# Optimization experiments

Measured on AMD Instinct MI355X. Metric: run time of the kernel, lower is better.

The kernel has to match this reference:

```python
import jax, jax.numpy as jnp
import numpy as np

B, N, D = 4, 2048, 1024
H = 16
HD = D // H


def setup_inputs() -> dict:
    key = jax.random.key(0)
    ks = jax.random.split(key, 7)
    bound_w = 1.0 / np.sqrt(D)  # kaiming_uniform(a=sqrt(5)) on (D, D) -> U(-1/sqrt(fan_in), 1/sqrt(fan_in))
    x = jax.random.normal(ks[0], (B, N, D), dtype=jnp.float32)
    Wq = jax.random.uniform(ks[1], (D, D), jnp.float32, -bound_w, bound_w)
    Wk = jax.random.uniform(ks[2], (D, D), jnp.float32, -bound_w, bound_w)
    Wv = jax.random.uniform(ks[3], (D, D), jnp.float32, -bound_w, bound_w)
    Wo = jax.random.uniform(ks[4], (D, D), jnp.float32, -bound_w, bound_w)
    bo = jax.random.uniform(ks[5], (D,), jnp.float32, -bound_w, bound_w)
    return {"x": x, "Wq": Wq, "Wk": Wk, "Wv": Wv, "Wo": Wo, "bo": bo}


def reference(x, Wq, Wk, Wv, Wo, bo):
    b, n, _ = x.shape
    # QKV projections: contraction over W's FIRST axis, matching torch einsum 'bnd,di->bni'
    Q = jnp.einsum('bnd,di->bni', x, Wq)
    K = jnp.einsum('bnd,di->bni', x, Wk)
    V = jnp.einsum('bnd,di->bni', x, Wv)
    # split heads: [b, h, n, hd]
    Q = Q.reshape(b, n, H, HD).transpose(0, 2, 1, 3)
    K = K.reshape(b, n, H, HD).transpose(0, 2, 1, 3)
    V = V.reshape(b, n, H, HD).transpose(0, 2, 1, 3)
    scores = jnp.einsum('bhnd,bhmd->bhnm', Q, K) / np.sqrt(HD).astype(np.float32)
    causal = jnp.triu(jnp.ones((n, n), dtype=bool), k=1)  # True above diagonal -> masked
    scores = jnp.where(causal[None, None, :, :], -jnp.inf, scores)
    attn = jax.nn.softmax(scores, axis=-1)
    # dropout rate is 0.0 -> identity
    ctx = jnp.einsum('bhnm,bhmd->bhnd', attn, V)
    ctx = ctx.transpose(0, 2, 1, 3).reshape(b, n, D)
    return ctx @ Wo.T + bo
```

## Files before the change

kernel.cpp:

```cpp
#include <hip/hip_runtime.h>
#include <hip/hip_bf16.h>

typedef __bf16 bf16;
typedef __bf16 bf16x4 __attribute__((ext_vector_type(4)));
typedef __bf16 bf16x8 __attribute__((ext_vector_type(8)));
typedef float  f32x4  __attribute__((ext_vector_type(4)));

#define B_  4
#define N_  2048
#define D_  1024
#define H_  16
#define HD_ 64

#define QSCALE 0.1803368801111204f

__device__ __forceinline__ bf16x8 ld8(const bf16* p) {
  return *reinterpret_cast<const bf16x8*>(p);
}
__device__ __forceinline__ float max3f(float a, float b, float c) {
  return fmaxf(fmaxf(a, b), c);
}

__device__ __forceinline__ void gload16(const bf16* g, bf16* l) {
  __builtin_amdgcn_global_load_lds(
      (const __attribute__((address_space(1))) void*)g,
      (__attribute__((address_space(3))) void*)l, 16, 0, 0);
}

__global__ __launch_bounds__(256) void cast_k(const float* __restrict__ in,
                                              bf16* __restrict__ out, int n) {
  int i = (blockIdx.x * 256 + threadIdx.x) * 8;
  if (i >= n) return;
  float4 a = *reinterpret_cast<const float4*>(in + i);
  float4 b = *reinterpret_cast<const float4*>(in + i + 4);
  bf16x8 o;
  o[0] = (bf16)a.x; o[1] = (bf16)a.y; o[2] = (bf16)a.z; o[3] = (bf16)a.w;
  o[4] = (bf16)b.x; o[5] = (bf16)b.y; o[6] = (bf16)b.z; o[7] = (bf16)b.w;
  *reinterpret_cast<bf16x8*>(out + i) = o;
}

__global__ __launch_bounds__(1024)
void transpose3_k(const float* __restrict__ w0, const float* __restrict__ w1,
                  const float* __restrict__ w2, bf16* __restrict__ out) {
  __shared__ float t[32][33];
  const int z = blockIdx.z;
  const float* in = (z == 0) ? w0 : (z == 1) ? w1 : w2;
  const float scale = (z == 0) ? QSCALE : 1.0f;
  bf16* o = out + (size_t)z * D_ * D_;
  int c = blockIdx.x * 32 + threadIdx.x;
  int r = blockIdx.y * 32 + threadIdx.y;
  t[threadIdx.y][threadIdx.x] = in[r * D_ + c];
  __syncthreads();
  int oc = blockIdx.y * 32 + threadIdx.x;
  int orr = blockIdx.x * 32 + threadIdx.y;
  o[orr * D_ + oc] = (bf16)(scale * t[threadIdx.x][threadIdx.y]);
}

#define GEMM_CORE(A_, Bt_, K_)                                                    \
  f32x4 acc[4][4] = {};                                                           \
  const int srow = wid * 16 + (lane >> 2);                \
  const int schk = ((lane & 3) ^ ((lane >> 4) & 3)) * 8;         \
  const int q8   = ((lane >> 4) ^ (l15 >> 2)) * 8;              \
  _Pragma("unroll")                                                               \
  for (int j = 0; j < 2; ++j) {                                                   \
    gload16(&(A_)[(size_t)(brow + j * 64 + srow) * (K_) + schk],                  \
            &As[(j * 64 + wid * 16) * 32]);                                       \
    gload16(&(Bt_)[(size_t)(bcol + j * 64 + srow) * (K_) + schk],                 \
            &Bs[(j * 64 + wid * 16) * 32]);                                       \
  }                                                                               \
  __syncthreads();                                                                \
  for (int kk = 0; kk < (K_); kk += 32) {                                         \
    const int cur = (kk >> 5) & 1;                                                \
    if (kk + 32 < (K_)) {                                                         \
      _Pragma("unroll")                                                           \
      for (int j = 0; j < 2; ++j) {                                               \
        gload16(&(A_)[(size_t)(brow + j * 64 + srow) * (K_) + kk + 32 + schk],    \
                &As[(cur ^ 1) * 4096 + (j * 64 + wid * 16) * 32]);                \
        gload16(&(Bt_)[(size_t)(bcol + j * 64 + srow) * (K_) + kk + 32 + schk],   \
                &Bs[(cur ^ 1) * 4096 + (j * 64 + wid * 16) * 32]);                \
      }                                                                           \
    }                                                                             \
    const bf16* Ac = &As[cur * 4096];                                             \
    const bf16* Bc = &Bs[cur * 4096];                                             \
    bf16x8 af[4], bfr[4];                                                         \
    _Pragma("unroll")                                                             \
    for (int m = 0; m < 4; ++m)                                                   \
      af[m] = *reinterpret_cast<const bf16x8*>(&Ac[(wr + m * 16 + l15) * 32 + q8]); \
    _Pragma("unroll")                                                             \
    for (int n = 0; n < 4; ++n)                                                   \
      bfr[n] = *reinterpret_cast<const bf16x8*>(&Bc[(wc + n * 16 + l15) * 32 + q8]); \
    _Pragma("unroll")                                                             \
    for (int m = 0; m < 4; ++m)                                                   \
      _Pragma("unroll")                                                           \
      for (int n = 0; n < 4; ++n)                                                 \
        acc[m][n] = __builtin_amdgcn_mfma_f32_16x16x32_bf16(af[m], bfr[n],        \
                                                            acc[m][n], 0, 0, 0);  \
    __syncthreads();                                                              \
  }

__global__ __launch_bounds__(256, 4)
void gemm_qkv(const bf16* __restrict__ A, const bf16* __restrict__ Bt,
              bf16* __restrict__ qb, bf16* __restrict__ kb, bf16* __restrict__ vtb)
{
  __shared__ bf16 As[2 * 128 * 32];
  __shared__ bf16 Bs[2 * 128 * 32];
  const int tid  = threadIdx.x;
  const int lane = tid & 63;
  const int wid  = tid >> 6;
  const int wg   = blockIdx.x;
  const int xcd  = wg & 7;
  const int idx  = wg >> 3;
  const int brow = ((xcd << 3) + (idx & 7)) * 128;
  const int bcol = (idx >> 3) * 128;
  const int wr   = (wid >> 1) * 64;
  const int wc   = (wid & 1) * 64;
  const int l15  = lane & 15;
  const int g    = lane >> 4;

  GEMM_CORE(A, Bt, D_)

  const int which = bcol >> 10;
  bf16* outp = (which == 0) ? qb : (which == 1) ? kb : vtb;
  const int r0 = g * 4;
#pragma unroll
  for (int m = 0; m < 4; ++m)
#pragma unroll
    for (int n = 0; n < 4; ++n)
#pragma unroll
      for (int r = 0; r < 4; ++r) {
        int grow = brow + wr + m * 16 + r0 + r;
        int gcol = (bcol & 1023) + wc + n * 16 + l15;
        int b = grow >> 11, nn = grow & (N_ - 1);
        int h = gcol >> 6, hd = gcol & 63;
        float v = acc[m][n][r];
        if (which == 2)
          outp[((size_t)((b * H_ + h) * HD_ + hd)) * N_ + nn] = (bf16)v;
        else
          outp[((((size_t)(b * H_ + h)) * N_ + nn) << 6) + hd] = (bf16)v;
      }
}

__global__ __launch_bounds__(256, 4)
void gemm_out(const bf16* __restrict__ A, const bf16* __restrict__ Bt,
              float* __restrict__ C, const float* __restrict__ bias)
{
  __shared__ bf16 As[2 * 128 * 32];
  __shared__ bf16 Bs[2 * 128 * 32];
  const int tid  = threadIdx.x;
  const int lane = tid & 63;
  const int wid  = tid >> 6;
  const int wg   = blockIdx.x;
  const int xcd  = wg & 7;
  const int idx  = wg >> 3;
  const int brow = ((xcd << 3) + (idx & 7)) * 128;
  const int bcol = (idx >> 3) * 128;
  const int wr   = (wid >> 1) * 64;
  const int wc   = (wid & 1) * 64;
  const int l15  = lane & 15;
  const int g    = lane >> 4;

  GEMM_CORE(A, Bt, D_)

  const int r0 = g * 4;
#pragma unroll
  for (int m = 0; m < 4; ++m)
#pragma unroll
    for (int n = 0; n < 4; ++n)
#pragma unroll
      for (int r = 0; r < 4; ++r) {
        int grow = brow + wr + m * 16 + r0 + r;
        int gcol = bcol + wc + n * 16 + l15;
        C[(size_t)grow * D_ + gcol] = acc[m][n][r] + bias[gcol];
      }
}

__global__ __launch_bounds__(256, 3)
void attn_k(const bf16* __restrict__ q, const bf16* __restrict__ k,
            const bf16* __restrict__ vt, bf16* __restrict__ ctx)
{
  __shared__ bf16 Ks[2][64 * 64];
  __shared__ bf16 Vs[2][64 * 64];
  __shared__ bf16 Pl[4][2][16][72];
  const int tid  = threadIdx.x;
  const int lane = tid & 63;
  const int wid  = tid >> 6;
  const int bid  = blockIdx.x;
  const int bh   = bid & 63;
  const int c    = 15 - (bid >> 6);
  const int l15  = lane & 15;
  const int g    = lane >> 4;
  const int lk   = g * 8;
  const int swz  = (l15 & 7) << 4;

  const bf16* kp = k  + (size_t)bh * N_ * HD_;
  const bf16* vp = vt + (size_t)bh * HD_ * N_;
  const int b = bh >> 4, h = bh & 15;

  const int sr8   = lane >> 3;
  const int scoff = ((lane & 7) ^ sr8) * 8;

  bf16x8 ones8;
#pragma unroll
  for (int i = 0; i < 8; ++i) ones8[i] = (bf16)1.0f;

  const int qbase = c * 128 + wid * 32;
  const int nt    = 2 * c + 2;
  const int tm    = 2 * c + (wid >> 1);

  const bf16* qp = q + ((size_t)bh * N_ + qbase) * HD_;
  bf16x8 aq[2][2];
#pragma unroll
  for (int m = 0; m < 2; ++m)
#pragma unroll
    for (int c2 = 0; c2 < 2; ++c2)
      aq[m][c2] = ld8(qp + (size_t)(m * 16 + l15) * HD_ + c2 * 32 + lk);

  float m_run[2] = {-1e30f, -1e30f};
  f32x4 oacc[2][5] = {};

#pragma unroll
  for (int j = 0; j < 2; ++j) {
    const int rr = j * 32 + wid * 8 + sr8;
    gload16(kp + (size_t)rr * HD_ + scoff, &Ks[0][(j * 32 + wid * 8) * 64]);
    gload16(vp + (size_t)rr * N_ + scoff, &Vs[0][(j * 32 + wid * 8) * 64]);
  }
  __syncthreads();

  for (int t = 0; t < nt; ++t) {
    const int cur = t & 1;
    if (t + 1 < nt) {
      const int kb = (t + 1) * 64;
#pragma unroll
      for (int j = 0; j < 2; ++j) {
        const int rr = j * 32 + wid * 8 + sr8;
        gload16(kp + (size_t)(kb + rr) * HD_ + scoff,
                &Ks[cur ^ 1][(j * 32 + wid * 8) * 64]);
        gload16(vp + (size_t)rr * N_ + kb + scoff,
                &Vs[cur ^ 1][(j * 32 + wid * 8) * 64]);
      }
    }
    if (t <= tm) {
      const char* kb_ = (const char*)&Ks[cur][0];
      const char* vb_ = (const char*)&Vs[cur][0];

      f32x4 s[2][4] = {};
#pragma unroll
      for (int tt = 0; tt < 4; ++tt) {
        bf16x8 bk0 = *reinterpret_cast<const bf16x8*>(
            kb_ + (tt * 16 + l15) * 128 + ((g * 16) ^ swz));
        bf16x8 bk1 = *reinterpret_cast<const bf16x8*>(
            kb_ + (tt * 16 + l15) * 128 + ((64 + g * 16) ^ swz));
#pragma unroll
        for (int m = 0; m < 2; ++m) {
          s[m][tt] = __builtin_amdgcn_mfma_f32_16x16x32_bf16(bk0, aq[m][0], s[m][tt], 0, 0, 0);
          s[m][tt] = __builtin_amdgcn_mfma_f32_16x16x32_bf16(bk1, aq[m][1], s[m][tt], 0, 0, 0);
        }
      }

      if (t == tm) {
#pragma unroll
        for (int m = 0; m < 2; ++m) {
          const int qr = qbase + m * 16 + l15;
#pragma unroll
          for (int tt = 0; tt < 4; ++tt)
#pragma unroll
            for (int r = 0; r < 4; ++r) {
              int kq = t * 64 + tt * 16 + g * 4 + r;
              if (kq > qr) s[m][tt][r] = -1e30f;
            }
        }
      }

#pragma unroll
      for (int m = 0; m < 2; ++m) {
        float pm = max3f(s[m][0][0], s[m][0][1], s[m][0][2]);
        pm = max3f(pm, s[m][0][3], s[m][1][0]);
        pm = max3f(pm, s[m][1][1], s[m][1][2]);
        pm = max3f(pm, s[m][1][3], s[m][2][0]);
        pm = max3f(pm, s[m][2][1], s[m][2][2]);
        pm = max3f(pm, s[m][2][3], s[m][3][0]);
        pm = max3f(pm, s[m][3][1], s[m][3][2]);
        pm = fmaxf(pm, s[m][3][3]);
        pm = fmaxf(pm, __shfl_xor(pm, 16));
        pm = fmaxf(pm, __shfl_xor(pm, 32));
        if (!__all(pm <= m_run[m] + 8.f)) {
          float mn = fmaxf(m_run[m], pm);
          float al = exp2f(m_run[m] - mn);
          m_run[m] = mn;
#pragma unroll
          for (int n = 0; n < 5; ++n)
#pragma unroll
            for (int r = 0; r < 4; ++r) oacc[m][n][r] *= al;
        }
#pragma unroll
        for (int tt = 0; tt < 4; ++tt)
#pragma unroll
          for (int r = 0; r < 4; ++r) s[m][tt][r] = exp2f(s[m][tt][r] - m_run[m]);

#pragma unroll
        for (int tt = 0; tt < 4; ++tt) {
          bf16x4 pk;
#pragma unroll
          for (int r = 0; r < 4; ++r) pk[r] = (bf16)s[m][tt][r];
          *reinterpret_cast<bf16x4*>(&Pl[wid][m][l15][tt * 16 + g * 4]) = pk;
        }
      }

#pragma unroll
      for (int kc = 0; kc < 2; ++kc) {
        bf16x8 pb[2];
#pragma unroll
        for (int m = 0; m < 2; ++m)
          pb[m] = *reinterpret_cast<const bf16x8*>(&Pl[wid][m][l15][kc * 32 + lk]);
#pragma unroll
        for (int n = 0; n < 4; ++n) {
          bf16x8 vf = *reinterpret_cast<const bf16x8*>(
              vb_ + (n * 16 + l15) * 128 + ((kc * 64 + g * 16) ^ swz));
#pragma unroll
          for (int m = 0; m < 2; ++m)
            oacc[m][n] = __builtin_amdgcn_mfma_f32_16x16x32_bf16(vf, pb[m], oacc[m][n], 0, 0, 0);
        }
#pragma unroll
        for (int m = 0; m < 2; ++m)
          oacc[m][4] = __builtin_amdgcn_mfma_f32_16x16x32_bf16(ones8, pb[m], oacc[m][4], 0, 0, 0);
      }
    }
    __syncthreads();
  }

#pragma unroll
  for (int m = 0; m < 2; ++m) {
    float inv = 1.f / oacc[m][4][0];
    bf16* cp = ctx + ((size_t)b * N_ + qbase + m * 16 + l15) * D_ + h * HD_;
#pragma unroll
    for (int n = 0; n < 4; ++n) {
      bf16x4 o;
#pragma unroll
      for (int r = 0; r < 4; ++r) o[r] = (bf16)(oacc[m][n][r] * inv);
      *reinterpret_cast<bf16x4*>(cp + n * 16 + g * 4) = o;
    }
  }
}

extern "C" void kernel_launch(void* const* d_in, const int* in_sizes, int n_in,
                              void* d_out, int out_size, void* d_ws, size_t ws_size,
                              hipStream_t stream)
{
  const float* x  = (const float*)d_in[0];
  const float* Wq = (const float*)d_in[1];
  const float* Wk = (const float*)d_in[2];
  const float* Wv = (const float*)d_in[3];
  const float* Wo = (const float*)d_in[4];
  const float* bo = (const float*)d_in[5];
  float* out = (float*)d_out;

  const size_t SZ_BHND = (size_t)B_ * H_ * N_ * HD_ * sizeof(bf16);
  const size_t SZ_W    = (size_t)D_ * D_ * sizeof(bf16);
  char* ws = (char*)d_ws;
  bf16* xbf  = (bf16*)(ws);
  bf16* ctx  = (bf16*)(ws);
  bf16* qb   = (bf16*)(ws + SZ_BHND);
  bf16* kbf  = (bf16*)(ws + 2 * SZ_BHND);
  bf16* vtb  = (bf16*)(ws + 3 * SZ_BHND);
  bf16* wqkv = (bf16*)(ws + 4 * SZ_BHND);
  bf16* wob  = (bf16*)(ws + 4 * SZ_BHND + 3 * SZ_W);
  if (ws_size < 4 * SZ_BHND + 4 * SZ_W) return;

  const int NX = B_ * N_ * D_;
  cast_k<<<NX / (256 * 8), 256, 0, stream>>>(x, xbf, NX);
  cast_k<<<(D_ * D_) / (256 * 8), 256, 0, stream>>>(Wo, wob, D_ * D_);

  transpose3_k<<<dim3(32, 32, 3), dim3(32, 32), 0, stream>>>(Wq, Wk, Wv, wqkv);

  gemm_qkv<<<1536, 256, 0, stream>>>(xbf, wqkv, qb, kbf, vtb);

  attn_k<<<1024, 256, 0, stream>>>(qb, kbf, vtb, ctx);

  gemm_out<<<512, 256, 0, stream>>>(ctx, wob, out, bo);
}
```

Before: 194.7 us.

## Use explicit barriers and partial vmcnt waits in GEMM loop; vectorize V^T stores

Replaces the __syncthreads-based double-buffer loop in the shared GEMM core with explicit s_barrier plus s_waitcnt vmcnt(4), so the next tile's global-to-LDS loads stay in flight while the current tile is computed. This is meant to cut synchronisation stalls in both the QKV and output projections. Separately, the transposed V epilogue now packs four consecutive rows into one bf16x4 store instead of four scalar stores. The hand-written waitcnt and barrier sequence relies on the load count and LDS visibility being exactly right, which risks races if that accounting is off.

```diff
diff --git a/kernel.cpp b/kernel.cpp
--- a/kernel.cpp
+++ b/kernel.cpp
@@ -68,18 +68,26 @@
     gload16(&(Bt_)[(size_t)(bcol + j * 64 + srow) * (K_) + schk],                 \
             &Bs[(j * 64 + wid * 16) * 32]);                                       \
   }                                                                               \
-  __syncthreads();                                                                \
-  for (int kk = 0; kk < (K_); kk += 32) {                                         \
-    const int cur = (kk >> 5) & 1;                                                \
-    if (kk + 32 < (K_)) {                                                         \
+  const int NIT = (K_) / 32;                                                      \
+  for (int t = 0; t < NIT; ++t) {                                                 \
+    const int cur = t & 1;                                                        \
+    asm volatile("s_barrier" ::: "memory");           \
+    __builtin_amdgcn_sched_barrier(0);                                            \
+    if (t + 1 < NIT) {                                                            \
+      const int kk = (t + 1) * 32;                                                \
       _Pragma("unroll")                                                           \
       for (int j = 0; j < 2; ++j) {                                               \
-        gload16(&(A_)[(size_t)(brow + j * 64 + srow) * (K_) + kk + 32 + schk],    \
+        gload16(&(A_)[(size_t)(brow + j * 64 + srow) * (K_) + kk + schk],         \
                 &As[(cur ^ 1) * 4096 + (j * 64 + wid * 16) * 32]);                \
-        gload16(&(Bt_)[(size_t)(bcol + j * 64 + srow) * (K_) + kk + 32 + schk],   \
+        gload16(&(Bt_)[(size_t)(bcol + j * 64 + srow) * (K_) + kk + schk],        \
                 &Bs[(cur ^ 1) * 4096 + (j * 64 + wid * 16) * 32]);                \
       }                                                                           \
+      asm volatile("s_waitcnt vmcnt(4)" ::: "memory");                            \
+    } else {                                                                      \
+      asm volatile("s_waitcnt vmcnt(0)" ::: "memory");                            \
     }                                                                             \
+    asm volatile("s_barrier" ::: "memory");             \
+    __builtin_amdgcn_sched_barrier(0);                                            \
     const bf16* Ac = &As[cur * 4096];                                             \
     const bf16* Bc = &Bs[cur * 4096];                                             \
     bf16x8 af[4], bfr[4];                                                         \
@@ -95,7 +103,6 @@
       for (int n = 0; n < 4; ++n)                                                 \
         acc[m][n] = __builtin_amdgcn_mfma_f32_16x16x32_bf16(af[m], bfr[n],        \
                                                             acc[m][n], 0, 0, 0);  \
-    __syncthreads();                                                              \
   }
 
 __global__ __launch_bounds__(256, 4)
@@ -120,24 +127,37 @@
   GEMM_CORE(A, Bt, D_)
 
   const int which = bcol >> 10;
-  bf16* outp = (which == 0) ? qb : (which == 1) ? kb : vtb;
   const int r0 = g * 4;
-#pragma unroll
-  for (int m = 0; m < 4; ++m)
-#pragma unroll
-    for (int n = 0; n < 4; ++n)
-#pragma unroll
-      for (int r = 0; r < 4; ++r) {
-        int grow = brow + wr + m * 16 + r0 + r;
+  if (which == 2) {
+#pragma unroll
+    for (int m = 0; m < 4; ++m)
+#pragma unroll
+      for (int n = 0; n < 4; ++n) {
+        int nn0  = brow + wr + m * 16 + r0;
         int gcol = (bcol & 1023) + wc + n * 16 + l15;
-        int b = grow >> 11, nn = grow & (N_ - 1);
+        int b = nn0 >> 11, nn = nn0 & (N_ - 1);
         int h = gcol >> 6, hd = gcol & 63;
-        float v = acc[m][n][r];
-        if (which == 2)
-          outp[((size_t)((b * H_ + h) * HD_ + hd)) * N_ + nn] = (bf16)v;
-        else
-          outp[((((size_t)(b * H_ + h)) * N_ + nn) << 6) + hd] = (bf16)v;
-      }
+        bf16x4 o;
+#pragma unroll
+        for (int r = 0; r < 4; ++r) o[r] = (bf16)acc[m][n][r];
+        *reinterpret_cast<bf16x4*>(
+            &vtb[((size_t)((b * H_ + h) * HD_ + hd)) * N_ + nn]) = o;
+      }
+  } else {
+    bf16* outp = (which == 0) ? qb : kb;
+#pragma unroll
+    for (int m = 0; m < 4; ++m)
+#pragma unroll
+      for (int n = 0; n < 4; ++n)
+#pragma unroll
+        for (int r = 0; r < 4; ++r) {
+          int grow = brow + wr + m * 16 + r0 + r;
+          int gcol = (bcol & 1023) + wc + n * 16 + l15;
+          int b = grow >> 11, nn = grow & (N_ - 1);
+          int h = gcol >> 6, hd = gcol & 63;
+          outp[((((size_t)(b * H_ + h)) * N_ + nn) << 6) + hd] = (bf16)acc[m][n][r];
+        }
+  }
 }
 
 __global__ __launch_bounds__(256, 4)
```

Measured after the change: 183.7 us. -5.7%, faster.
